# Kernel optimization log

Hardware: AMD Instinct MI355X
Metric: run time of the kernel (lower is better)

## Reference

```python
import jax, jax.numpy as jnp
import numpy as np

N = 50000      # nodes
E = 600000     # directed edges
F_IN = 11      # node features (QM9-like)
G = 512        # graphs in batch
TGT = 12


def _lin(key, fi, fo):
    kw, kb = jax.random.split(key)
    s = 1.0 / np.sqrt(fi)
    W = jax.random.uniform(kw, (fi, fo), jnp.float32, -s, s)
    b = jax.random.uniform(kb, (fo,), jnp.float32, -s, s)
    return W, b


def setup_inputs() -> dict:
    key = jax.random.key(0)
    ks = jax.random.split(key, 9)
    x = jax.random.normal(ks[0], (N, F_IN), jnp.float32)
    edge_index = jax.random.randint(ks[1], (2, E), 0, N, dtype=jnp.int32)
    batch = jnp.sort(jax.random.randint(ks[2], (N,), 0, G, dtype=jnp.int32))
    W1, b1 = _lin(ks[3], F_IN, 32)
    W2, b2 = _lin(ks[4], 32, 64)
    W3, b3 = _lin(ks[5], 64, 128)
    fw1, fb1 = _lin(ks[6], 128, 64)
    fw2, fb2 = _lin(ks[7], 64, TGT)
    return {"x": x, "edge_index": edge_index, "batch": batch,
            "W1": W1, "b1": b1, "W2": W2, "b2": b2, "W3": W3, "b3": b3,
            "fw1": fw1, "fb1": fb1, "fw2": fw2, "fb2": fb2}


def reference(x, edge_index, batch, W1, b1, W2, b2, W3, b3, fw1, fb1, fw2, fb2):
    src, dst = edge_index[0], edge_index[1]
    n = x.shape[0]
    # GCN symmetric normalization with self-loops: deg counts incoming edges + 1
    deg = 1.0 + jax.ops.segment_sum(jnp.ones(src.shape[0], x.dtype), dst, num_segments=n)
    dis = jax.lax.rsqrt(deg)                      # deg^{-1/2}, [N]
    edge_norm = dis[src] * dis[dst]               # [E]

    def gcn_conv(h, W, b):
        hw = h @ W                                # [N, Fo]
        agg = jax.ops.segment_sum(hw[src] * edge_norm[:, None], dst, num_segments=n)
        # self-loop contribution: deg^{-1} * hw
        return agg + hw * (dis * dis)[:, None] + b

    h = jax.nn.relu(gcn_conv(x, W1, b1))
    h = jax.nn.relu(gcn_conv(h, W2, b2))
    h = gcn_conv(h, W3, b3)                       # no relu before pooling (matches source)

    # global_mean_pool over batch ids
    sums = jax.ops.segment_sum(h, batch, num_segments=G)
    counts = jax.ops.segment_sum(jnp.ones(n, h.dtype), batch, num_segments=G)
    pooled = sums / jnp.maximum(counts, 1.0)[:, None]

    h = jax.nn.relu(pooled @ fw1 + fb1)
    return h @ fw2 + fb2
```

## Files before the change

### kernel.cpp

```cpp
#include <hip/hip_runtime.h>
#include <hip/hip_fp16.h>


#define GG 512
#define TGT 12

union F4H8 { float4 f4; __half2 h2[4]; };

__device__ __forceinline__ void acc_add_h8(float* a, float4 raw) {
    F4H8 u; u.f4 = raw;
#pragma unroll
    for (int k = 0; k < 4; ++k) {
        float2 f = __half22float2(u.h2[k]);
        a[2 * k] += f.x;
        a[2 * k + 1] += f.y;
    }
}

__global__ void zero_kernel(int4* __restrict__ p, int n4) {
    int i = blockIdx.x * blockDim.x + threadIdx.x;
    if (i < n4) p[i] = make_int4(0, 0, 0, 0);
}

__global__ void deg_count_kernel(const int* __restrict__ dst, int* __restrict__ cnt, int E) {
    int i = blockIdx.x * blockDim.x + threadIdx.x;
    if (i < E) atomicAdd(&cnt[dst[i]], 1);
}


__global__ void prep_kernel(const int* __restrict__ cnt, const float* __restrict__ x,
                            float* __restrict__ dis, float* __restrict__ hs,
                            int* __restrict__ excl, int* __restrict__ psum, int n, int nb1) {
    int gid = blockIdx.x * 256 + threadIdx.x;
    int gstride = gridDim.x * 256;
    for (int idx = gid; idx < n * 16; idx += gstride) {
        int node = idx >> 4, lane = idx & 15;
        float d = rsqrtf(1.0f + (float)cnt[node]);
        if (lane == 0) dis[node] = d;
        hs[idx] = (lane < 11) ? x[node * 11 + lane] * d : 0.0f;
    }
    if (blockIdx.x < nb1) {
        __shared__ int sh[256];
        int i = blockIdx.x * 256 + threadIdx.x;
        int v = (i < n) ? cnt[i] : 0;
        sh[threadIdx.x] = v;
        __syncthreads();
        for (int off = 1; off < 256; off <<= 1) {
            int t = (threadIdx.x >= (unsigned)off) ? sh[threadIdx.x - off] : 0;
            __syncthreads();
            sh[threadIdx.x] += t;
            __syncthreads();
        }
        if (i < n) excl[i] = sh[threadIdx.x] - v;
        if (threadIdx.x == 255) psum[blockIdx.x] = sh[255];
    }
}

__global__ void scan2_kernel(int* __restrict__ psum, int nb) {
    __shared__ int sh[256];
    int carry = 0;
    for (int base = 0; base < nb; base += 256) {
        int i = base + threadIdx.x;
        int v = (i < nb) ? psum[i] : 0;
        sh[threadIdx.x] = v;
        __syncthreads();
        for (int off = 1; off < 256; off <<= 1) {
            int t = (threadIdx.x >= (unsigned)off) ? sh[threadIdx.x - off] : 0;
            __syncthreads();
            sh[threadIdx.x] += t;
            __syncthreads();
        }
        if (i < nb) psum[i] = sh[threadIdx.x] - v + carry;
        carry += sh[255];
        __syncthreads();
    }
}

__global__ void place_kernel(const int* __restrict__ src, const int* __restrict__ dst,
                             const int* __restrict__ excl, const int* __restrict__ psum,
                             int* __restrict__ incnt, int* __restrict__ esrc, int E) {
    int i = blockIdx.x * blockDim.x + threadIdx.x;
    if (i < E) {
        int d = dst[i];
        int r = atomicSub(&incnt[d], 1) - 1;
        esrc[excl[d] + psum[d >> 8] + r] = src[i];
    }
}

__device__ __forceinline__ int offs_of(const int* __restrict__ excl,
                                       const int* __restrict__ psum, int i) {
    return excl[i] + psum[i >> 8];
}


__global__ void aggemm1_kernel(const float4* __restrict__ hp, const float* __restrict__ dis,
                               const int* __restrict__ excl, const int* __restrict__ psum,
                               const int* __restrict__ esrc,
                               const float* __restrict__ W, const float* __restrict__ b,
                               __half* __restrict__ out, int n, int Etot) {
    __shared__ float srow[64 * 16];
    __shared__ float sdn[64];
    __shared__ float sW[11 * 32];
    for (int i = threadIdx.x; i < 11 * 32; i += 256) sW[i] = W[i];

    int nd = threadIdx.x >> 2, lane = threadIdx.x & 3;
    int node = blockIdx.x * 64 + nd;
    if (node < n) {
        int s0 = offs_of(excl, psum, node);
        int send = (node + 1 < n) ? offs_of(excl, psum, node + 1) : Etot;
        int c = send - s0;
        float4 A = hp[(size_t)node * 4 + lane];
        float4 B = make_float4(0, 0, 0, 0);
        int e = 0;
        for (; e + 4 <= c; e += 4) {
            int sa = esrc[s0 + e], sb = esrc[s0 + e + 1];
            int sc = esrc[s0 + e + 2], sd = esrc[s0 + e + 3];
            float4 va = hp[(size_t)sa * 4 + lane], vb = hp[(size_t)sb * 4 + lane];
            float4 vc = hp[(size_t)sc * 4 + lane], vd = hp[(size_t)sd * 4 + lane];
            A.x += va.x + vb.x; A.y += va.y + vb.y; A.z += va.z + vb.z; A.w += va.w + vb.w;
            B.x += vc.x + vd.x; B.y += vc.y + vd.y; B.z += vc.z + vd.z; B.w += vc.w + vd.w;
        }
        for (; e < c; ++e) {
            float4 va = hp[(size_t)esrc[s0 + e] * 4 + lane];
            A.x += va.x; A.y += va.y; A.z += va.z; A.w += va.w;
        }
        float dn = dis[node];
        srow[nd * 16 + lane * 4 + 0] = (A.x + B.x) * dn;
        srow[nd * 16 + lane * 4 + 1] = (A.y + B.y) * dn;
        srow[nd * 16 + lane * 4 + 2] = (A.z + B.z) * dn;
        srow[nd * 16 + lane * 4 + 3] = (A.w + B.w) * dn;
        if (lane == 0) sdn[nd] = dn;
    }
    __syncthreads();

    int base = blockIdx.x * 64;
    for (int o = threadIdx.x; o < 64 * 32; o += 256) {
        int fo = o & 31, nd2 = o >> 5;
        int node2 = base + nd2;
        if (node2 < n) {
            float a = b[fo];
#pragma unroll
            for (int fi = 0; fi < 11; ++fi) a += srow[nd2 * 16 + fi] * sW[fi * 32 + fo];
            out[(size_t)node2 * 32 + fo] = __float2half(fmaxf(a, 0.0f) * sdn[nd2]);
        }
    }
}


__global__ void aggemm2_kernel(const float4* __restrict__ hp, const float* __restrict__ dis,
                               const int* __restrict__ excl, const int* __restrict__ psum,
                               const int* __restrict__ esrc,
                               const float* __restrict__ W, const float* __restrict__ b,
                               __half* __restrict__ out, int n, int Etot) {
    __shared__ float srow[64 * 32];
    __shared__ float sdn[64];
    __shared__ float sW[32 * 64];
    for (int i = threadIdx.x; i < 32 * 64; i += 256) sW[i] = W[i];

    int nd = threadIdx.x >> 2, lane = threadIdx.x & 3;
    int node = blockIdx.x * 64 + nd;
    if (node < n) {
        int s0 = offs_of(excl, psum, node);
        int send = (node + 1 < n) ? offs_of(excl, psum, node + 1) : Etot;
        int c = send - s0;
        float accA[8] = {0, 0, 0, 0, 0, 0, 0, 0};
        float accB[8] = {0, 0, 0, 0, 0, 0, 0, 0};
        acc_add_h8(accA, hp[(size_t)node * 4 + lane]);
        int e = 0;
        for (; e + 4 <= c; e += 4) {
            int sa = esrc[s0 + e], sb = esrc[s0 + e + 1];
            int sc = esrc[s0 + e + 2], sd = esrc[s0 + e + 3];
            float4 va = hp[(size_t)sa * 4 + lane], vb = hp[(size_t)sb * 4 + lane];
            float4 vc = hp[(size_t)sc * 4 + lane], vd = hp[(size_t)sd * 4 + lane];
            acc_add_h8(accA, va); acc_add_h8(accB, vb);
            acc_add_h8(accA, vc); acc_add_h8(accB, vd);
        }
        for (; e < c; ++e) acc_add_h8(accA, hp[(size_t)esrc[s0 + e] * 4 + lane]);
        float dn = dis[node];
#pragma unroll
        for (int j = 0; j < 8; ++j) srow[nd * 32 + lane * 8 + j] = (accA[j] + accB[j]) * dn;
        if (lane == 0) sdn[nd] = dn;
    }
    __syncthreads();

    int base = blockIdx.x * 64;
    for (int o = threadIdx.x; o < 64 * 64; o += 256) {
        int fo = o & 63, nd2 = o >> 6;
        int node2 = base + nd2;
        if (node2 < n) {
            float a = b[fo];
#pragma unroll
            for (int fi = 0; fi < 32; ++fi) a += srow[nd2 * 32 + fi] * sW[fi * 64 + fo];
            out[(size_t)node2 * 64 + fo] = __float2half(fmaxf(a, 0.0f) * sdn[nd2]);
        }
    }
}


__global__ void agg64pool_kernel(const float4* __restrict__ hp, const float* __restrict__ dis,
                                 const int* __restrict__ excl, const int* __restrict__ psum,
                                 const int* __restrict__ esrc, const int* __restrict__ batch,
                                 float* __restrict__ pooled, int n, int Etot) {
    __shared__ float srow[32 * 64];
    int nd = threadIdx.x >> 3, lane = threadIdx.x & 7;
    int base = blockIdx.x * 32;
    int node = base + nd;
    if (node < n) {
        int s0 = offs_of(excl, psum, node);
        int send = (node + 1 < n) ? offs_of(excl, psum, node + 1) : Etot;
        int c = send - s0;
        float accA[8] = {0, 0, 0, 0, 0, 0, 0, 0};
        float accB[8] = {0, 0, 0, 0, 0, 0, 0, 0};
        acc_add_h8(accA, hp[(size_t)node * 8 + lane]);
        int e = 0;
        for (; e + 4 <= c; e += 4) {
            int sa = esrc[s0 + e], sb = esrc[s0 + e + 1];
            int sc = esrc[s0 + e + 2], sd = esrc[s0 + e + 3];
            float4 va = hp[(size_t)sa * 8 + lane], vb = hp[(size_t)sb * 8 + lane];
            float4 vc = hp[(size_t)sc * 8 + lane], vd = hp[(size_t)sd * 8 + lane];
            acc_add_h8(accA, va); acc_add_h8(accB, vb);
            acc_add_h8(accA, vc); acc_add_h8(accB, vd);
        }
        for (; e < c; ++e) acc_add_h8(accA, hp[(size_t)esrc[s0 + e] * 8 + lane]);
        float dn = dis[node];
#pragma unroll
        for (int j = 0; j < 8; ++j) srow[nd * 64 + lane * 8 + j] = (accA[j] + accB[j]) * dn;
    } else {
#pragma unroll
        for (int j = 0; j < 8; ++j) srow[nd * 64 + lane * 8 + j] = 0.0f;
    }
    __syncthreads();

    int fo = threadIdx.x & 63, q = threadIdx.x >> 6;
    float acc = 0.0f;
    int gcur = -1;
    for (int k = 0; k < 8; ++k) {
        int node2 = base + q * 8 + k;
        if (node2 >= n) break;
        int g = batch[node2];
        if (g != gcur) {
            if (gcur >= 0) atomicAdd(&pooled[(size_t)gcur * 64 + fo], acc);
            acc = 0.0f;
            gcur = g;
        }
        acc += srow[(q * 8 + k) * 64 + fo];
    }
    if (gcur >= 0) atomicAdd(&pooled[(size_t)gcur * 64 + fo], acc);
}


__global__ void head_kernel(const float* __restrict__ pooled, const int* __restrict__ batch,
                            const float* __restrict__ W3, const float* __restrict__ b3,
                            const float* __restrict__ fw1, const float* __restrict__ fb1,
                            const float* __restrict__ fw2, const float* __restrict__ fb2,
                            float* __restrict__ out, int n) {
    int g = blockIdx.x;
    auto lb = [&](int key) {
        int lo = 0, hi = n;
        while (lo < hi) {
            int mid = (lo + hi) >> 1;
            if (batch[mid] < key) lo = mid + 1; else hi = mid;
        }
        return lo;
    };
    int lo = lb(g), hi = lb(g + 1);
    float c = (float)(hi - lo);
    float inv = (c > 0.0f) ? 1.0f / c : 0.0f;

    __shared__ float sp[64];
    __shared__ float p128[128];
    __shared__ float h64[64];
    int j = threadIdx.x;
    if (j < 64) sp[j] = pooled[(size_t)g * 64 + j] * inv;
    __syncthreads();
    {
        float a = (c > 0.0f) ? b3[j] : 0.0f;
#pragma unroll
        for (int k = 0; k < 64; ++k) a += sp[k] * W3[k * 128 + j];
        p128[j] = a;
    }
    __syncthreads();
    if (j < 64) {
        float a = fb1[j];
#pragma unroll
        for (int k = 0; k < 128; ++k) a += p128[k] * fw1[k * 64 + j];
        h64[j] = fmaxf(a, 0.0f);
    }
    __syncthreads();
    if (j < TGT) {
        float a = fb2[j];
#pragma unroll
        for (int k = 0; k < 64; ++k) a += h64[k] * fw2[k * TGT + j];
        out[(size_t)g * TGT + j] = a;
    }
}

extern "C" void kernel_launch(void* const* d_in, const int* in_sizes, int n_in,
                              void* d_out, int out_size, void* d_ws, size_t ws_size,
                              hipStream_t stream) {
    const float* x = (const float*)d_in[0];
    const int* edge_index = (const int*)d_in[1];
    const int* batch = (const int*)d_in[2];
    const float* W1 = (const float*)d_in[3];
    const float* b1 = (const float*)d_in[4];
    const float* W2 = (const float*)d_in[5];
    const float* b2 = (const float*)d_in[6];
    const float* W3 = (const float*)d_in[7];
    const float* b3 = (const float*)d_in[8];
    const float* fw1 = (const float*)d_in[9];
    const float* fb1 = (const float*)d_in[10];
    const float* fw2 = (const float*)d_in[11];
    const float* fb2 = (const float*)d_in[12];
    float* out = (float*)d_out;

    const int N = in_sizes[2];
    const int E = in_sizes[1] / 2;
    const int* src = edge_index;
    const int* dst = edge_index + E;

    int* incnt = (int*)d_ws;
    float* pooled = (float*)(incnt + N);
    int* excl = (int*)(pooled + GG * 64);
    int* psum = excl + N;
    int* esrc = psum + 256;
    float* dis = (float*)(esrc + E);
    float* hx = dis + N;
    __half* h1 = (__half*)(hx + (size_t)N * 16);
    __half* h2 = h1 + (size_t)N * 32;

    const int T = 256;
    auto cdiv = [](long long a, long long b) { return (int)((a + b - 1) / b); };
    const int nb1 = cdiv(N, 256);

    const int zero_ints = N + GG * 64;
    zero_kernel<<<cdiv(cdiv(zero_ints, 4), T), T, 0, stream>>>((int4*)d_ws, cdiv(zero_ints, 4));
    deg_count_kernel<<<cdiv(E, T), T, 0, stream>>>(dst, incnt, E);
    prep_kernel<<<cdiv((long long)N * 16, T), T, 0, stream>>>(incnt, x, dis, hx, excl, psum, N, nb1);
    scan2_kernel<<<1, 256, 0, stream>>>(psum, nb1);
    place_kernel<<<cdiv(E, T), T, 0, stream>>>(src, dst, excl, psum, incnt, esrc, E);

    aggemm1_kernel<<<cdiv(N, 64), T, 0, stream>>>(
        (const float4*)hx, dis, excl, psum, esrc, W1, b1, h1, N, E);
    aggemm2_kernel<<<cdiv(N, 64), T, 0, stream>>>(
        (const float4*)h1, dis, excl, psum, esrc, W2, b2, h2, N, E);
    agg64pool_kernel<<<cdiv(N, 32), T, 0, stream>>>(
        (const float4*)h2, dis, excl, psum, esrc, batch, pooled, N, E);
    head_kernel<<<GG, 128, 0, stream>>>(pooled, batch, W3, b3, fw1, fb1, fw2, fb2, out, N);
}
```

Baseline: 138.3 us.

## Store layer-1 input in fp16, fuse scan into prep, split 64-wide aggregation

The layer-1 input features are now stored as fp16, which halves the gather traffic in the first aggregation. The second-level scan kernel is folded into prep_kernel through a last-block-done atomic counter, removing one launch. Layer-2 output is written as two 32-feature halves so the final aggregate-and-pool runs as two passes over narrower 64-byte rows, aiming for a smaller gather footprint and better cache locality. In exchange the edge list is walked twice, fp16 rounding is added on the input features, and pooling issues more atomics.

```diff
diff --git a/kernel.cpp b/kernel.cpp
--- a/kernel.cpp
+++ b/kernel.cpp
@@ -6,6 +6,7 @@
 #define TGT 12
 
 union F4H8 { float4 f4; __half2 h2[4]; };
+union F2H4 { float2 f2; __half2 h2[2]; };
 
 __device__ __forceinline__ void acc_add_h8(float* a, float4 raw) {
     F4H8 u; u.f4 = raw;
@@ -17,6 +18,16 @@
     }
 }
 
+__device__ __forceinline__ void acc_add_h4(float* a, float2 raw) {
+    F2H4 u; u.f2 = raw;
+#pragma unroll
+    for (int k = 0; k < 2; ++k) {
+        float2 f = __half22float2(u.h2[k]);
+        a[2 * k] += f.x;
+        a[2 * k + 1] += f.y;
+    }
+}
+
 __global__ void zero_kernel(int4* __restrict__ p, int n4) {
     int i = blockIdx.x * blockDim.x + threadIdx.x;
     if (i < n4) p[i] = make_int4(0, 0, 0, 0);
@@ -29,18 +40,20 @@
 
 
 __global__ void prep_kernel(const int* __restrict__ cnt, const float* __restrict__ x,
-                            float* __restrict__ dis, float* __restrict__ hs,
-                            int* __restrict__ excl, int* __restrict__ psum, int n, int nb1) {
+                            float* __restrict__ dis, __half* __restrict__ hx,
+                            int* __restrict__ excl, int* __restrict__ psum,
+                            int* __restrict__ done, int n, int nb1) {
     int gid = blockIdx.x * 256 + threadIdx.x;
     int gstride = gridDim.x * 256;
     for (int idx = gid; idx < n * 16; idx += gstride) {
         int node = idx >> 4, lane = idx & 15;
         float d = rsqrtf(1.0f + (float)cnt[node]);
         if (lane == 0) dis[node] = d;
-        hs[idx] = (lane < 11) ? x[node * 11 + lane] * d : 0.0f;
-    }
-    if (blockIdx.x < nb1) {
-        __shared__ int sh[256];
+        hx[idx] = __float2half((lane < 11) ? x[node * 11 + lane] * d : 0.0f);
+    }
+    __shared__ int sh[256];
+    __shared__ int islast;
+    if ((int)blockIdx.x < nb1) {
         int i = blockIdx.x * 256 + threadIdx.x;
         int v = (i < n) ? cnt[i] : 0;
         sh[threadIdx.x] = v;
@@ -54,25 +67,31 @@
         if (i < n) excl[i] = sh[threadIdx.x] - v;
         if (threadIdx.x == 255) psum[blockIdx.x] = sh[255];
     }
-}
-
-__global__ void scan2_kernel(int* __restrict__ psum, int nb) {
-    __shared__ int sh[256];
-    int carry = 0;
-    for (int base = 0; base < nb; base += 256) {
-        int i = base + threadIdx.x;
-        int v = (i < nb) ? psum[i] : 0;
-        sh[threadIdx.x] = v;
-        __syncthreads();
-        for (int off = 1; off < 256; off <<= 1) {
-            int t = (threadIdx.x >= (unsigned)off) ? sh[threadIdx.x - off] : 0;
+    __syncthreads();
+    if (threadIdx.x == 0) {
+        __threadfence();
+        int old = __hip_atomic_fetch_add(done, 1, __ATOMIC_ACQ_REL, __HIP_MEMORY_SCOPE_AGENT);
+        islast = (old == (int)gridDim.x - 1) ? 1 : 0;
+    }
+    __syncthreads();
+    if (islast) {
+        __threadfence();
+        int carry = 0;
+        for (int base = 0; base < nb1; base += 256) {
+            int i = base + threadIdx.x;
+            int v = (i < nb1) ? psum[i] : 0;
+            sh[threadIdx.x] = v;
             __syncthreads();
-            sh[threadIdx.x] += t;
+            for (int off = 1; off < 256; off <<= 1) {
+                int t = (threadIdx.x >= (unsigned)off) ? sh[threadIdx.x - off] : 0;
+                __syncthreads();
+                sh[threadIdx.x] += t;
+                __syncthreads();
+            }
+            if (i < nb1) psum[i] = sh[threadIdx.x] - v + carry;
+            carry += sh[255];
             __syncthreads();
         }
-        if (i < nb) psum[i] = sh[threadIdx.x] - v + carry;
-        carry += sh[255];
-        __syncthreads();
     }
 }
 
@@ -93,7 +112,7 @@
 }
 
 
-__global__ void aggemm1_kernel(const float4* __restrict__ hp, const float* __restrict__ dis,
+__global__ void aggemm1_kernel(const float2* __restrict__ hp, const float* __restrict__ dis,
                                const int* __restrict__ excl, const int* __restrict__ psum,
                                const int* __restrict__ esrc,
                                const float* __restrict__ W, const float* __restrict__ b,
@@ -109,26 +128,22 @@
         int s0 = offs_of(excl, psum, node);
         int send = (node + 1 < n) ? offs_of(excl, psum, node + 1) : Etot;
         int c = send - s0;
-        float4 A = hp[(size_t)node * 4 + lane];
-        float4 B = make_float4(0, 0, 0, 0);
+        float accA[4] = {0, 0, 0, 0};
+        float accB[4] = {0, 0, 0, 0};
+        acc_add_h4(accA, hp[(size_t)node * 4 + lane]);
         int e = 0;
         for (; e + 4 <= c; e += 4) {
             int sa = esrc[s0 + e], sb = esrc[s0 + e + 1];
             int sc = esrc[s0 + e + 2], sd = esrc[s0 + e + 3];
-            float4 va = hp[(size_t)sa * 4 + lane], vb = hp[(size_t)sb * 4 + lane];
-            float4 vc = hp[(size_t)sc * 4 + lane], vd = hp[(size_t)sd * 4 + lane];
-            A.x += va.x + vb.x; A.y += va.y + vb.y; A.z += va.z + vb.z; A.w += va.w + vb.w;
-            B.x += vc.x + vd.x; B.y += vc.y + vd.y; B.z += vc.z + vd.z; B.w += vc.w + vd.w;
-        }
-        for (; e < c; ++e) {
-            float4 va = hp[(size_t)esrc[s0 + e] * 4 + lane];
-            A.x += va.x; A.y += va.y; A.z += va.z; A.w += va.w;
-        }
+            float2 va = hp[(size_t)sa * 4 + lane], vb = hp[(size_t)sb * 4 + lane];
+            float2 vc = hp[(size_t)sc * 4 + lane], vd = hp[(size_t)sd * 4 + lane];
+            acc_add_h4(accA, va); acc_add_h4(accB, vb);
+            acc_add_h4(accA, vc); acc_add_h4(accB, vd);
+        }
+        for (; e < c; ++e) acc_add_h4(accA, hp[(size_t)esrc[s0 + e] * 4 + lane]);
         float dn = dis[node];
-        srow[nd * 16 + lane * 4 + 0] = (A.x + B.x) * dn;
-        srow[nd * 16 + lane * 4 + 1] = (A.y + B.y) * dn;
-        srow[nd * 16 + lane * 4 + 2] = (A.z + B.z) * dn;
-        srow[nd * 16 + lane * 4 + 3] = (A.w + B.w) * dn;
+#pragma unroll
+        for (int j = 0; j < 4; ++j) srow[nd * 16 + lane * 4 + j] = (accA[j] + accB[j]) * dn;
         if (lane == 0) sdn[nd] = dn;
     }
     __syncthreads();
@@ -151,7 +166,8 @@
                                const int* __restrict__ excl, const int* __restrict__ psum,
                                const int* __restrict__ esrc,
                                const float* __restrict__ W, const float* __restrict__ b,
-                               __half* __restrict__ out, int n, int Etot) {
+                               __half* __restrict__ out_a, __half* __restrict__ out_b,
+                               int n, int Etot) {
     __shared__ float srow[64 * 32];
     __shared__ float sdn[64];
     __shared__ float sW[32 * 64];
@@ -191,19 +207,21 @@
             float a = b[fo];
 #pragma unroll
             for (int fi = 0; fi < 32; ++fi) a += srow[nd2 * 32 + fi] * sW[fi * 64 + fo];
-            out[(size_t)node2 * 64 + fo] = __float2half(fmaxf(a, 0.0f) * sdn[nd2]);
-        }
-    }
-}
-
-
-__global__ void agg64pool_kernel(const float4* __restrict__ hp, const float* __restrict__ dis,
+            __half v = __float2half(fmaxf(a, 0.0f) * sdn[nd2]);
+            __half* o32 = (fo < 32) ? out_a : out_b;
+            o32[(size_t)node2 * 32 + (fo & 31)] = v;
+        }
+    }
+}
+
+
+__global__ void agg32pool_kernel(const float4* __restrict__ hp, const float* __restrict__ dis,
                                  const int* __restrict__ excl, const int* __restrict__ psum,
                                  const int* __restrict__ esrc, const int* __restrict__ batch,
-                                 float* __restrict__ pooled, int n, int Etot) {
-    __shared__ float srow[32 * 64];
-    int nd = threadIdx.x >> 3, lane = threadIdx.x & 7;
-    int base = blockIdx.x * 32;
+                                 float* __restrict__ pooledHalf, int n, int Etot) {
+    __shared__ float srow[64 * 32];
+    int nd = threadIdx.x >> 2, lane = threadIdx.x & 3;
+    int base = blockIdx.x * 64;
     int node = base + nd;
     if (node < n) {
         int s0 = offs_of(excl, psum, node);
@@ -211,27 +229,27 @@
         int c = send - s0;
         float accA[8] = {0, 0, 0, 0, 0, 0, 0, 0};
         float accB[8] = {0, 0, 0, 0, 0, 0, 0, 0};
-        acc_add_h8(accA, hp[(size_t)node * 8 + lane]);
+        acc_add_h8(accA, hp[(size_t)node * 4 + lane]);
         int e = 0;
         for (; e + 4 <= c; e += 4) {
             int sa = esrc[s0 + e], sb = esrc[s0 + e + 1];
             int sc = esrc[s0 + e + 2], sd = esrc[s0 + e + 3];
-            float4 va = hp[(size_t)sa * 8 + lane], vb = hp[(size_t)sb * 8 + lane];
-            float4 vc = hp[(size_t)sc * 8 + lane], vd = hp[(size_t)sd * 8 + lane];
+            float4 va = hp[(size_t)sa * 4 + lane], vb = hp[(size_t)sb * 4 + lane];
+            float4 vc = hp[(size_t)sc * 4 + lane], vd = hp[(size_t)sd * 4 + lane];
             acc_add_h8(accA, va); acc_add_h8(accB, vb);
             acc_add_h8(accA, vc); acc_add_h8(accB, vd);
         }
-        for (; e < c; ++e) acc_add_h8(accA, hp[(size_t)esrc[s0 + e] * 8 + lane]);
+        for (; e < c; ++e) acc_add_h8(accA, hp[(size_t)esrc[s0 + e] * 4 + lane]);
         float dn = dis[node];
 #pragma unroll
-        for (int j = 0; j < 8; ++j) srow[nd * 64 + lane * 8 + j] = (accA[j] + accB[j]) * dn;
+        for (int j = 0; j < 8; ++j) srow[nd * 32 + lane * 8 + j] = (accA[j] + accB[j]) * dn;
     } else {
 #pragma unroll
-        for (int j = 0; j < 8; ++j) srow[nd * 64 + lane * 8 + j] = 0.0f;
-    }
-    __syncthreads();
-
-    int fo = threadIdx.x & 63, q = threadIdx.x >> 6;
+        for (int j = 0; j < 8; ++j) srow[nd * 32 + lane * 8 + j] = 0.0f;
+    }
+    __syncthreads();
+
+    int fo = threadIdx.x & 31, q = threadIdx.x >> 5;
     float acc = 0.0f;
     int gcur = -1;
     for (int k = 0; k < 8; ++k) {
@@ -239,13 +257,13 @@
         if (node2 >= n) break;
         int g = batch[node2];
         if (g != gcur) {
-            if (gcur >= 0) atomicAdd(&pooled[(size_t)gcur * 64 + fo], acc);
+            if (gcur >= 0) atomicAdd(&pooledHalf[(size_t)gcur * 64 + fo], acc);
             acc = 0.0f;
             gcur = g;
         }
-        acc += srow[(q * 8 + k) * 64 + fo];
-    }
-    if (gcur >= 0) atomicAdd(&pooled[(size_t)gcur * 64 + fo], acc);
+        acc += srow[(q * 8 + k) * 32 + fo];
+    }
+    if (gcur >= 0) atomicAdd(&pooledHalf[(size_t)gcur * 64 + fo], acc);
 }
 
 
@@ -320,30 +338,34 @@
 
     int* incnt = (int*)d_ws;
     float* pooled = (float*)(incnt + N);
-    int* excl = (int*)(pooled + GG * 64);
+    int* done = (int*)(pooled + GG * 64);
+    int* excl = done + 16;
     int* psum = excl + N;
     int* esrc = psum + 256;
     float* dis = (float*)(esrc + E);
-    float* hx = dis + N;
-    __half* h1 = (__half*)(hx + (size_t)N * 16);
-    __half* h2 = h1 + (size_t)N * 32;
+    __half* hx = (__half*)(dis + N);
+    __half* h1 = hx + (size_t)N * 16;
+    __half* h2a = h1 + (size_t)N * 32;
+    __half* h2b = h2a + (size_t)N * 32;
 
     const int T = 256;
     auto cdiv = [](long long a, long long b) { return (int)((a + b - 1) / b); };
     const int nb1 = cdiv(N, 256);
 
-    const int zero_ints = N + GG * 64;
+    const int zero_ints = N + GG * 64 + 16;
     zero_kernel<<<cdiv(cdiv(zero_ints, 4), T), T, 0, stream>>>((int4*)d_ws, cdiv(zero_ints, 4));
     deg_count_kernel<<<cdiv(E, T), T, 0, stream>>>(dst, incnt, E);
-    prep_kernel<<<cdiv((long long)N * 16, T), T, 0, stream>>>(incnt, x, dis, hx, excl, psum, N, nb1);
-    scan2_kernel<<<1, 256, 0, stream>>>(psum, nb1);
+    prep_kernel<<<cdiv((long long)N * 16, T), T, 0, stream>>>(incnt, x, dis, hx, excl, psum,
+                                                              done, N, nb1);
     place_kernel<<<cdiv(E, T), T, 0, stream>>>(src, dst, excl, psum, incnt, esrc, E);
 
     aggemm1_kernel<<<cdiv(N, 64), T, 0, stream>>>(
-        (const float4*)hx, dis, excl, psum, esrc, W1, b1, h1, N, E);
+        (const float2*)hx, dis, excl, psum, esrc, W1, b1, h1, N, E);
     aggemm2_kernel<<<cdiv(N, 64), T, 0, stream>>>(
-        (const float4*)h1, dis, excl, psum, esrc, W2, b2, h2, N, E);
-    agg64pool_kernel<<<cdiv(N, 32), T, 0, stream>>>(
-        (const float4*)h2, dis, excl, psum, esrc, batch, pooled, N, E);
+        (const float4*)h1, dis, excl, psum, esrc, W2, b2, h2a, h2b, N, E);
+    agg32pool_kernel<<<cdiv(N, 64), T, 0, stream>>>(
+        (const float4*)h2a, dis, excl, psum, esrc, batch, pooled, N, E);
+    agg32pool_kernel<<<cdiv(N, 64), T, 0, stream>>>(
+        (const float4*)h2b, dis, excl, psum, esrc, batch, pooled + 32, N, E);
     head_kernel<<<GG, 128, 0, stream>>>(pooled, batch, W3, b3, fw1, fb1, fw2, fb2, out, N);
 }
```

New measurement: 242.2 us. 75.2% more time.
